# Kernel optimization log

Measured on AMD Instinct MI355X. Metric: run time of the kernel, lower is better.

Reference implementation:

```python
import jax, jax.numpy as jnp
import numpy as np

N = 128       # batch (hard-coded in the torch module)
NEG = 112     # negatives per anchor (N - 16 per-class samples)
HALF = 56
MARGIN = 0.3
EPS = 1e-12
D = 2048


def _pair_dist(x, y):
    xx = jnp.sum(x * x, axis=1, keepdims=True)          # [m,1]
    yy = jnp.sum(y * y, axis=1, keepdims=True).T        # [1,n]
    d2 = xx + yy - 2.0 * (x @ y.T)
    return jnp.sqrt(jnp.maximum(d2, EPS))


def _row_dist(a, b):
    # diagonal of euclidean_dist(a, b): per-row distance, same clamp/sqrt
    d2 = jnp.sum(a * a, axis=1) + jnp.sum(b * b, axis=1) - 2.0 * jnp.sum(a * b, axis=1)
    return jnp.sqrt(jnp.maximum(d2, EPS))


def setup_inputs() -> dict:
    key = jax.random.key(0)
    k1, k2 = jax.random.split(key)
    global_feat1 = jax.random.normal(k1, (N, D), dtype=jnp.float32)
    global_feat2 = jax.random.normal(k2, (N, D), dtype=jnp.float32)
    # PK-sampled labels: 8 identities x 8 samples, duplicated across two modalities
    # -> exactly 16 positives / 112 negatives per anchor (required by the hard-coded views)
    labels = jnp.repeat(jnp.arange(8, dtype=jnp.int64), 8)
    target = jnp.tile(labels, 2)  # [128]
    return {"global_feat1": global_feat1, "global_feat2": global_feat2, "target": target}


def reference(global_feat1, global_feat2, target):
    dist_mat = _pair_dist(global_feat1, global_feat2)           # [N,N]
    is_pos = target[None, :] == target[:, None]                 # [N,N]

    # hard_example_mining: hardest positive / hardest negative per anchor
    dist_ap = jnp.max(jnp.where(is_pos, dist_mat, -jnp.inf), axis=1)  # [N]

    # negative column indices per row, in ascending column order (matches
    # torch boolean-mask row-major flattening). Stable argsort: False (neg) first.
    neg_idx = jnp.argsort(is_pos.astype(jnp.int32), axis=1, stable=True)[:, :NEG]  # [N,112]
    dist_neg = jnp.take_along_axis(dist_mat, neg_idx, axis=1)                      # [N,112]

    # per-row top-1 smallest negative in each 56-half (the 128-iter torch loop)
    i1 = jnp.argmin(dist_neg[:, :HALF], axis=1)          # [N]
    i2 = jnp.argmin(dist_neg[:, HALF:], axis=1) + HALF   # [N]
    r = jnp.arange(N)
    sel1 = neg_idx[r, i1]
    sel2 = neg_idx[r, i2]
    # mean of the two selected hard negatives (features taken from global_feat1)
    feat_mean = 0.5 * (global_feat1[sel1] + global_feat1[sel2])  # [N,D]

    c0, c1, c2, c3 = jnp.split(feat_mean, 4, axis=0)
    feat_rgb_mid = jnp.concatenate([c0, c2], axis=0)             # [64,D]
    feat_ir_mid = jnp.concatenate([c1, c3], axis=0)              # [64,D]

    H = N // 2
    feat_rgb = jnp.concatenate([global_feat1[:H], global_feat2[:H]], axis=0)  # [128,D]
    feat_ir = jnp.concatenate([global_feat1[H:], global_feat2[H:]], axis=0)   # [128,D]

    # torch.diag of a [128,64] matrix keeps only the first 64 diagonal entries
    d_rgb = _row_dist(feat_rgb[:64], feat_rgb_mid)   # [64]
    d_ir = _row_dist(feat_ir[:64], feat_ir_mid)      # [64]
    dist_an = jnp.concatenate([d_rgb, d_ir], axis=0)  # [128]

    triplets = dist_ap - dist_an + MARGIN
    pos_mask = triplets > 0
    loss = jnp.sum(jnp.where(pos_mask, triplets, 0.0)) / 128.0
    num_active = jnp.sum(pos_mask.astype(jnp.int32))
    return loss, num_active
```

## Files before the change

kernel.cpp:

```cpp
#include <hip/hip_runtime.h>
#include <math.h>

#define NN 128
#define DD 2048
#define LDSTR 132

__device__ __forceinline__ float waveReduceSum(float v) {
#pragma unroll
  for (int o = 32; o > 0; o >>= 1) v += __shfl_down(v, o, 64);
  return v;
}

__global__ __launch_bounds__(256) void k_fused(const float* __restrict__ f1,
                                               const float* __restrict__ f2,
                                               unsigned* __restrict__ flags1,
                                               unsigned* __restrict__ flags2,
                                               float* __restrict__ tripv,
                                               float* __restrict__ dbuf,
                                               float* __restrict__ out) {
  __shared__ float s1[32 * LDSTR];
  __shared__ float s2[32 * LDSTR];
  __shared__ unsigned long long sg0[2], sg1[2];
  __shared__ float spos[2];
  __shared__ int ssel[2];
  __shared__ float sap;
  __shared__ float sred[4];
  __shared__ float fv[4], fa[4];

  const int b = blockIdx.x;
  const int t = threadIdx.x;
  const int lane = t & 63;
  const int wv = t >> 6;

  {
    const int i0 = (b & 3) * 32;
    const int j0 = ((b >> 2) & 3) * 32;
    const int kc = (b >> 4) * 128;

    const int row = t >> 3;
    const int c0 = (t & 7) * 4;
    const float* p1 = f1 + (size_t)(i0 + row) * DD + kc;
    const float* p2 = f2 + (size_t)(j0 + row) * DD + kc;
#pragma unroll
    for (int u = 0; u < 4; ++u) {
      const int c = c0 + 32 * u;
      *(float4*)&s1[row * LDSTR + c] = *(const float4*)(p1 + c);
      *(float4*)&s2[row * LDSTR + c] = *(const float4*)(p2 + c);
    }
    __syncthreads();

    const int ii = t >> 4;
    const int jj = t & 15;
    float a00 = 0.f, a01 = 0.f, a10 = 0.f, a11 = 0.f;
#pragma unroll 4
    for (int k = 0; k < 128; k += 4) {
      float4 x0 = *(const float4*)&s1[ii * LDSTR + k];
      float4 x1 = *(const float4*)&s1[(ii + 16) * LDSTR + k];
      float4 y0 = *(const float4*)&s2[jj * LDSTR + k];
      float4 y1 = *(const float4*)&s2[jj * LDSTR + k + 16 * LDSTR];
#define STEP(C)                                          \
      {                                                  \
        float d0 = x0.C - y0.C; a00 = fmaf(d0, d0, a00); \
        float d1 = x0.C - y1.C; a01 = fmaf(d1, d1, a01); \
        float dv = x1.C - y0.C; a10 = fmaf(dv, dv, a10); \
        float d3 = x1.C - y1.C; a11 = fmaf(d3, d3, a11); \
      }
      STEP(x) STEP(y) STEP(z) STEP(w)
#undef STEP
    }

    float* dst = dbuf + (size_t)(b >> 4) * NN * NN;
    dst[(i0 + ii) * NN + (j0 + jj)] = a00;
    dst[(i0 + ii) * NN + (j0 + jj + 16)] = a01;
    dst[(i0 + ii + 16) * NN + (j0 + jj)] = a10;
    dst[(i0 + ii + 16) * NN + (j0 + jj + 16)] = a11;

    __syncthreads();
    if (t == 0) {
      __threadfence();
      __hip_atomic_store(&flags1[b], 0x5A5A0000u | (unsigned)b,
                         __ATOMIC_RELEASE, __HIP_MEMORY_SCOPE_AGENT);
    }
  }

  if (b >= NN) return;

  {
    const unsigned exp1 = 0x5A5A0000u | (unsigned)t;
    while (__hip_atomic_load(&flags1[t], __ATOMIC_ACQUIRE,
                             __HIP_MEMORY_SCOPE_AGENT) != exp1) {
      __builtin_amdgcn_s_sleep(1);
    }
  }
  __syncthreads();

  const int k = b;
  int m = k;
  if (k >= 32 && k < 64) m = k + 32;
  else if (k >= 64 && k < 96) m = k - 32;

  const int j = t & 127;
  const int rrow = (t < 128) ? m : k;
  float v = 0.f;
#pragma unroll
  for (int p = 0; p < 16; ++p) v += dbuf[p * NN * NN + rrow * NN + j];

  if (t < 128) {
    const int L8 = ((m & 63) >> 3) * 8;
    const bool isneg = (((j & 63) >> 3) != ((m & 63) >> 3));
    int c1 = j - L8;        c1 = c1 < 0 ? 0 : (c1 > 8 ? 8 : c1);
    int c2 = j - (64 + L8); c2 = c2 < 0 ? 0 : (c2 > 8 ? 8 : c2);
    const int negc = j - c1 - c2;
    const unsigned long long key =
        ((unsigned long long)__float_as_uint(v) << 32) | (unsigned)j;
    unsigned long long k0 = (isneg && negc < 56) ? key : ~0ull;
    unsigned long long k1 = (isneg && negc >= 56) ? key : ~0ull;
#pragma unroll
    for (int o = 32; o > 0; o >>= 1) {
      unsigned long long o0 = __shfl_down(k0, o, 64);
      unsigned long long o1 = __shfl_down(k1, o, 64);
      k0 = o0 < k0 ? o0 : k0;
      k1 = o1 < k1 ? o1 : k1;
    }
    if (lane == 0) { sg0[wv] = k0; sg1[wv] = k1; }
  } else {
    const bool ispos = (((j & 63) >> 3) == ((k & 63) >> 3));
    float pv = ispos ? v : -1.f;
#pragma unroll
    for (int o = 32; o > 0; o >>= 1) pv = fmaxf(pv, __shfl_down(pv, o, 64));
    if (lane == 0) spos[wv - 2] = pv;
  }
  __syncthreads();
  if (t == 0) {
    const unsigned long long b0 = sg0[0] < sg0[1] ? sg0[0] : sg0[1];
    const unsigned long long b1 = sg1[0] < sg1[1] ? sg1[0] : sg1[1];
    ssel[0] = (int)(unsigned)(b0 & 0xffffffffu);
    ssel[1] = (int)(unsigned)(b1 & 0xffffffffu);
    const float apv = fmaxf(spos[0], spos[1]);
    sap = sqrtf(fmaxf(apv, 1e-12f));
  }
  __syncthreads();

  const int sa_ = ssel[0], sb_ = ssel[1];
  const float4* pk = (const float4*)(f1 + (size_t)k * DD);
  const float4* pa = (const float4*)(f1 + (size_t)sa_ * DD);
  const float4* pb = (const float4*)(f1 + (size_t)sb_ * DD);
  float acc = 0.f;
#pragma unroll
  for (int it = 0; it < 2; ++it) {
    const int idx = it * 256 + t;
    float4 xk = pk[idx];
    float4 xa = pa[idx];
    float4 xb = pb[idx];
    float d;
    d = xk.x - 0.5f * (xa.x + xb.x); acc = fmaf(d, d, acc);
    d = xk.y - 0.5f * (xa.y + xb.y); acc = fmaf(d, d, acc);
    d = xk.z - 0.5f * (xa.z + xb.z); acc = fmaf(d, d, acc);
    d = xk.w - 0.5f * (xa.w + xb.w); acc = fmaf(d, d, acc);
  }
  acc = waveReduceSum(acc);
  if (lane == 0) sred[wv] = acc;
  __syncthreads();
  if (t == 0) {
    const float d2v = sred[0] + sred[1] + sred[2] + sred[3];
    const float dan = sqrtf(fmaxf(d2v, 1e-12f));
    const float trip = sap - dan + 0.3f;
    tripv[k] = trip;
    __threadfence();
    __hip_atomic_store(&flags2[k], 0x5A5B0000u | (unsigned)k,
                       __ATOMIC_RELEASE, __HIP_MEMORY_SCOPE_AGENT);
  }

  if (b != 0) return;

  float tv = 0.f, av = 0.f;
  if (t < NN) {
    const unsigned exp2 = 0x5A5B0000u | (unsigned)t;
    while (__hip_atomic_load(&flags2[t], __ATOMIC_ACQUIRE,
                             __HIP_MEMORY_SCOPE_AGENT) != exp2) {
      __builtin_amdgcn_s_sleep(1);
    }
    const float x = tripv[t];
    tv = x > 0.f ? x : 0.f;
    av = x > 0.f ? 1.f : 0.f;
  }
  tv = waveReduceSum(tv);
  av = waveReduceSum(av);
  if (lane == 0) { fv[wv] = tv; fa[wv] = av; }
  __syncthreads();
  if (t == 0) {
    out[0] = (fv[0] + fv[1] + fv[2] + fv[3]) * (1.f / 128.f);
    out[1] = fa[0] + fa[1] + fa[2] + fa[3];
  }
}

extern "C" void kernel_launch(void* const* d_in, const int* in_sizes, int n_in,
                              void* d_out, int out_size, void* d_ws, size_t ws_size,
                              hipStream_t stream) {
  const float* f1 = (const float*)d_in[0];
  const float* f2 = (const float*)d_in[1];

  unsigned* flags1 = (unsigned*)d_ws;
  unsigned* flags2 = flags1 + 256;
  float* tripv = (float*)(flags2 + 128);
  float* dbuf = (float*)d_ws + 1024;

  k_fused<<<256, 256, 0, stream>>>(f1, f2, flags1, flags2, tripv, dbuf,
                                   (float*)d_out);
}
```

Measured before the change: 83.44 us.

## Compute only needed distance rows per block and drop grid-wide split-K barrier

```diff
diff --git a/kernel.cpp b/kernel.cpp
--- a/kernel.cpp
+++ b/kernel.cpp
@@ -3,7 +3,6 @@
 
 #define NN 128
 #define DD 2048
-#define LDSTR 132
 
 __device__ __forceinline__ float waveReduceSum(float v) {
 #pragma unroll
@@ -11,124 +10,100 @@
   return v;
 }
 
-__global__ __launch_bounds__(256) void k_fused(const float* __restrict__ f1,
-                                               const float* __restrict__ f2,
-                                               unsigned* __restrict__ flags1,
-                                               unsigned* __restrict__ flags2,
-                                               float* __restrict__ tripv,
-                                               float* __restrict__ dbuf,
-                                               float* __restrict__ out) {
-  __shared__ float s1[32 * LDSTR];
-  __shared__ float s2[32 * LDSTR];
+__global__ __launch_bounds__(512) void k_all(const float* __restrict__ f1,
+                                             const float* __restrict__ f2,
+                                             unsigned* __restrict__ flags,
+                                             float* __restrict__ tripv,
+                                             float* __restrict__ out) {
+  __shared__ float s1[2 * DD];
+  __shared__ float pda[512];
+  __shared__ float pdb[512];
   __shared__ unsigned long long sg0[2], sg1[2];
   __shared__ float spos[2];
   __shared__ int ssel[2];
   __shared__ float sap;
-  __shared__ float sred[4];
-  __shared__ float fv[4], fa[4];
+  __shared__ float sred[8];
+  __shared__ float fv[8], fa[8];
 
-  const int b = blockIdx.x;
+  const int k = blockIdx.x;
+  int m = k;
+  if (k >= 32 && k < 64) m = k + 32;
+  else if (k >= 64 && k < 96) m = k - 32;
+
   const int t = threadIdx.x;
   const int lane = t & 63;
   const int wv = t >> 6;
 
   {
-    const int i0 = (b & 3) * 32;
-    const int j0 = ((b >> 2) & 3) * 32;
-    const int kc = (b >> 4) * 128;
-
-    const int row = t >> 3;
-    const int c0 = (t & 7) * 4;
-    const float* p1 = f1 + (size_t)(i0 + row) * DD + kc;
-    const float* p2 = f2 + (size_t)(j0 + row) * DD + kc;
-#pragma unroll
-    for (int u = 0; u < 4; ++u) {
-      const int c = c0 + 32 * u;
-      *(float4*)&s1[row * LDSTR + c] = *(const float4*)(p1 + c);
-      *(float4*)&s2[row * LDSTR + c] = *(const float4*)(p2 + c);
-    }
-    __syncthreads();
-
-    const int ii = t >> 4;
-    const int jj = t & 15;
-    float a00 = 0.f, a01 = 0.f, a10 = 0.f, a11 = 0.f;
-#pragma unroll 4
-    for (int k = 0; k < 128; k += 4) {
-      float4 x0 = *(const float4*)&s1[ii * LDSTR + k];
-      float4 x1 = *(const float4*)&s1[(ii + 16) * LDSTR + k];
-      float4 y0 = *(const float4*)&s2[jj * LDSTR + k];
-      float4 y1 = *(const float4*)&s2[jj * LDSTR + k + 16 * LDSTR];
-#define STEP(C)                                          \
-      {                                                  \
-        float d0 = x0.C - y0.C; a00 = fmaf(d0, d0, a00); \
-        float d1 = x0.C - y1.C; a01 = fmaf(d1, d1, a01); \
-        float dv = x1.C - y0.C; a10 = fmaf(dv, dv, a10); \
-        float d3 = x1.C - y1.C; a11 = fmaf(d3, d3, a11); \
-      }
-      STEP(x) STEP(y) STEP(z) STEP(w)
-#undef STEP
-    }
-
-    float* dst = dbuf + (size_t)(b >> 4) * NN * NN;
-    dst[(i0 + ii) * NN + (j0 + jj)] = a00;
-    dst[(i0 + ii) * NN + (j0 + jj + 16)] = a01;
-    dst[(i0 + ii + 16) * NN + (j0 + jj)] = a10;
-    dst[(i0 + ii + 16) * NN + (j0 + jj + 16)] = a11;
-
-    __syncthreads();
-    if (t == 0) {
-      __threadfence();
-      __hip_atomic_store(&flags1[b], 0x5A5A0000u | (unsigned)b,
-                         __ATOMIC_RELEASE, __HIP_MEMORY_SCOPE_AGENT);
-    }
-  }
-
-  if (b >= NN) return;
-
-  {
-    const unsigned exp1 = 0x5A5A0000u | (unsigned)t;
-    while (__hip_atomic_load(&flags1[t], __ATOMIC_ACQUIRE,
-                             __HIP_MEMORY_SCOPE_AGENT) != exp1) {
-      __builtin_amdgcn_s_sleep(1);
-    }
+    const float4* pk4 = (const float4*)(f1 + (size_t)k * DD);
+    const float4* pm4 = (const float4*)(f1 + (size_t)m * DD);
+    float4* s4 = (float4*)s1;
+    s4[t] = pk4[t];
+    s4[t + 512] = pm4[t];
   }
   __syncthreads();
 
-  const int k = b;
-  int m = k;
-  if (k >= 32 && k < 64) m = k + 32;
-  else if (k >= 64 && k < 96) m = k - 32;
+  {
+    const int j = t & 127;
+    const int kh = t >> 7;
+    const float4* pf2 = (const float4*)(f2 + (size_t)j * DD) + kh * 128;
+    const float4* xk4 = (const float4*)s1 + kh * 128;
+    const float4* xm4 = (const float4*)(s1 + DD) + kh * 128;
+    float ak = 0.f, am = 0.f;
+#pragma unroll 8
+    for (int i = 0; i < 128; ++i) {
+      float4 bq = pf2[i];
+      float4 xk = xk4[i];
+      float4 xm = xm4[i];
+      float d;
+      d = xk.x - bq.x; ak = fmaf(d, d, ak);
+      d = xm.x - bq.x; am = fmaf(d, d, am);
+      d = xk.y - bq.y; ak = fmaf(d, d, ak);
+      d = xm.y - bq.y; am = fmaf(d, d, am);
+      d = xk.z - bq.z; ak = fmaf(d, d, ak);
+      d = xm.z - bq.z; am = fmaf(d, d, am);
+      d = xk.w - bq.w; ak = fmaf(d, d, ak);
+      d = xm.w - bq.w; am = fmaf(d, d, am);
+    }
+    pda[t] = ak;
+    pdb[t] = am;
+  }
+  __syncthreads();
 
-  const int j = t & 127;
-  const int rrow = (t < 128) ? m : k;
-  float v = 0.f;
+  if (t < 256) {
+    const int j = t & 127;
+    float v;
+    if (t < 128) {
+      v = pdb[j] + pdb[j + 128] + pdb[j + 256] + pdb[j + 384];
+    } else {
+      v = pda[j] + pda[j + 128] + pda[j + 256] + pda[j + 384];
+    }
+
+    if (t < 128) {
+      const int L8 = ((m & 63) >> 3) * 8;
+      const bool isneg = (((j & 63) >> 3) != ((m & 63) >> 3));
+      int c1 = j - L8;        c1 = c1 < 0 ? 0 : (c1 > 8 ? 8 : c1);
+      int c2 = j - (64 + L8); c2 = c2 < 0 ? 0 : (c2 > 8 ? 8 : c2);
+      const int negc = j - c1 - c2;
+      const unsigned long long key =
+          ((unsigned long long)__float_as_uint(v) << 32) | (unsigned)j;
+      unsigned long long k0 = (isneg && negc < 56) ? key : ~0ull;
+      unsigned long long k1 = (isneg && negc >= 56) ? key : ~0ull;
 #pragma unroll
-  for (int p = 0; p < 16; ++p) v += dbuf[p * NN * NN + rrow * NN + j];
-
-  if (t < 128) {
-    const int L8 = ((m & 63) >> 3) * 8;
-    const bool isneg = (((j & 63) >> 3) != ((m & 63) >> 3));
-    int c1 = j - L8;        c1 = c1 < 0 ? 0 : (c1 > 8 ? 8 : c1);
-    int c2 = j - (64 + L8); c2 = c2 < 0 ? 0 : (c2 > 8 ? 8 : c2);
-    const int negc = j - c1 - c2;
-    const unsigned long long key =
-        ((unsigned long long)__float_as_uint(v) << 32) | (unsigned)j;
-    unsigned long long k0 = (isneg && negc < 56) ? key : ~0ull;
-    unsigned long long k1 = (isneg && negc >= 56) ? key : ~0ull;
+      for (int o = 32; o > 0; o >>= 1) {
+        unsigned long long o0 = __shfl_down(k0, o, 64);
+        unsigned long long o1 = __shfl_down(k1, o, 64);
+        k0 = o0 < k0 ? o0 : k0;
+        k1 = o1 < k1 ? o1 : k1;
+      }
+      if (lane == 0) { sg0[wv] = k0; sg1[wv] = k1; }
+    } else {
+      const bool ispos = (((j & 63) >> 3) == ((k & 63) >> 3));
+      float pv = ispos ? v : -1.f;
 #pragma unroll
-    for (int o = 32; o > 0; o >>= 1) {
-      unsigned long long o0 = __shfl_down(k0, o, 64);
-      unsigned long long o1 = __shfl_down(k1, o, 64);
-      k0 = o0 < k0 ? o0 : k0;
-      k1 = o1 < k1 ? o1 : k1;
+      for (int o = 32; o > 0; o >>= 1) pv = fmaxf(pv, __shfl_down(pv, o, 64));
+      if (lane == 0) spos[wv - 2] = pv;
     }
-    if (lane == 0) { sg0[wv] = k0; sg1[wv] = k1; }
-  } else {
-    const bool ispos = (((j & 63) >> 3) == ((k & 63) >> 3));
-    float pv = ispos ? v : -1.f;
-#pragma unroll
-    for (int o = 32; o > 0; o >>= 1) pv = fmaxf(pv, __shfl_down(pv, o, 64));
-    if (lane == 0) spos[wv - 2] = pv;
   }
   __syncthreads();
   if (t == 0) {
@@ -141,45 +116,47 @@
   }
   __syncthreads();
 
-  const int sa_ = ssel[0], sb_ = ssel[1];
-  const float4* pk = (const float4*)(f1 + (size_t)k * DD);
-  const float4* pa = (const float4*)(f1 + (size_t)sa_ * DD);
-  const float4* pb = (const float4*)(f1 + (size_t)sb_ * DD);
-  float acc = 0.f;
-#pragma unroll
-  for (int it = 0; it < 2; ++it) {
-    const int idx = it * 256 + t;
-    float4 xk = pk[idx];
-    float4 xa = pa[idx];
-    float4 xb = pb[idx];
-    float d;
+  {
+    const int sa_ = ssel[0], sb_ = ssel[1];
+    const float4* pa4 = (const float4*)(f1 + (size_t)sa_ * DD);
+    const float4* pb4 = (const float4*)(f1 + (size_t)sb_ * DD);
+    float4 xk = ((const float4*)s1)[t];
+    float4 xa = pa4[t];
+    float4 xb = pb4[t];
+    float acc = 0.f, d;
     d = xk.x - 0.5f * (xa.x + xb.x); acc = fmaf(d, d, acc);
     d = xk.y - 0.5f * (xa.y + xb.y); acc = fmaf(d, d, acc);
     d = xk.z - 0.5f * (xa.z + xb.z); acc = fmaf(d, d, acc);
     d = xk.w - 0.5f * (xa.w + xb.w); acc = fmaf(d, d, acc);
+    acc = waveReduceSum(acc);
+    if (lane == 0) sred[wv] = acc;
   }
-  acc = waveReduceSum(acc);
-  if (lane == 0) sred[wv] = acc;
   __syncthreads();
   if (t == 0) {
-    const float d2v = sred[0] + sred[1] + sred[2] + sred[3];
+    float d2v = 0.f;
+#pragma unroll
+    for (int w = 0; w < 8; ++w) d2v += sred[w];
     const float dan = sqrtf(fmaxf(d2v, 1e-12f));
     const float trip = sap - dan + 0.3f;
     tripv[k] = trip;
     __threadfence();
-    __hip_atomic_store(&flags2[k], 0x5A5B0000u | (unsigned)k,
+    __hip_atomic_store(&flags[k], 0x5A5C0000u | (unsigned)k,
                        __ATOMIC_RELEASE, __HIP_MEMORY_SCOPE_AGENT);
   }
 
-  if (b != 0) return;
+  if (k != 0) return;
 
+  if (t < NN) {
+    const unsigned exp = 0x5A5C0000u | (unsigned)t;
+    while (__hip_atomic_load(&flags[t], __ATOMIC_RELAXED,
+                             __HIP_MEMORY_SCOPE_AGENT) != exp) {
+      __builtin_amdgcn_s_sleep(1);
+    }
+  }
+  __syncthreads();
+  __threadfence();
   float tv = 0.f, av = 0.f;
   if (t < NN) {
-    const unsigned exp2 = 0x5A5B0000u | (unsigned)t;
-    while (__hip_atomic_load(&flags2[t], __ATOMIC_ACQUIRE,
-                             __HIP_MEMORY_SCOPE_AGENT) != exp2) {
-      __builtin_amdgcn_s_sleep(1);
-    }
     const float x = tripv[t];
     tv = x > 0.f ? x : 0.f;
     av = x > 0.f ? 1.f : 0.f;
@@ -189,8 +166,11 @@
   if (lane == 0) { fv[wv] = tv; fa[wv] = av; }
   __syncthreads();
   if (t == 0) {
-    out[0] = (fv[0] + fv[1] + fv[2] + fv[3]) * (1.f / 128.f);
-    out[1] = fa[0] + fa[1] + fa[2] + fa[3];
+    float L = 0.f, A = 0.f;
+#pragma unroll
+    for (int w = 0; w < 8; ++w) { L += fv[w]; A += fa[w]; }
+    out[0] = L * (1.f / 128.f);
+    out[1] = A;
   }
 }
 
@@ -200,11 +180,8 @@
   const float* f1 = (const float*)d_in[0];
   const float* f2 = (const float*)d_in[1];
 
-  unsigned* flags1 = (unsigned*)d_ws;
-  unsigned* flags2 = flags1 + 256;
-  float* tripv = (float*)(flags2 + 128);
-  float* dbuf = (float*)d_ws + 1024;
+  unsigned* flags = (unsigned*)d_ws;
+  float* tripv = (float*)d_ws + 256;
 
-  k_fused<<<256, 256, 0, stream>>>(f1, f2, flags1, flags2, tripv, dbuf,
-                                   (float*)d_out);
+  k_all<<<NN, 512, 0, stream>>>(f1, f2, flags, tripv, (float*)d_out);
 }
```

New measurement: 93.41 us. 11.9% more time.
